# Kernel optimization log

Hardware: AMD Instinct MI355X
Metric: run time of the kernel (lower is better)

The kernel has to match this reference:

```python
import jax, jax.numpy as jnp
import numpy as np

OUT, IN, RANK = 4096, 4096, 1024
B, T = 4, 4096

def setup_inputs() -> dict:
    key = jax.random.key(0)
    kx, ku, ks, kv = jax.random.split(key, 4)
    x = jax.random.normal(kx, (B, T, IN), dtype=jnp.float32)
    # Orthonormal-ish factors scaled like SVD outputs
    U = jax.random.normal(ku, (OUT, RANK), dtype=jnp.float32) / np.sqrt(OUT)
    S = jax.random.uniform(ks, (RANK,), dtype=jnp.float32, minval=0.1, maxval=10.0)
    S = jnp.sort(S)[::-1]  # descending singular values
    V = jax.random.normal(kv, (IN, RANK), dtype=jnp.float32) / np.sqrt(IN)
    return {"x": x, "U": U, "S": S, "V": V}

def reference(x, U, S, V):
    # Faithful to torch: weight = U @ diag(S) @ V.T  (shape [out, in]),
    # then F.linear(x, weight) = x @ weight.T
    weight = (U * S[None, :]) @ V.T          # [out, in]
    return jnp.einsum('bti,oi->bto', x, weight)
```

## Files before the change

kernel.cpp:

```cpp
#include <hip/hip_runtime.h>


typedef __bf16 bf16;
typedef __bf16 bf16x4 __attribute__((ext_vector_type(4)));
typedef __bf16 bf16x8 __attribute__((ext_vector_type(8)));
typedef float  f32x4  __attribute__((ext_vector_type(4)));

#define M_DIM   16384
#define IN_DIM  4096
#define OUT_DIM 4096
#define RK_DIM  1024

__global__ __launch_bounds__(256)
void prep_kernel(const float* __restrict__ x, const float* __restrict__ U,
                 const float* __restrict__ S, const float* __restrict__ V,
                 bf16* __restrict__ xb, bf16* __restrict__ Ub,
                 bf16* __restrict__ VsT, int xblocks)
{
    __shared__ float tile[64][68];
    const int b = blockIdx.x;
    const int tid = threadIdx.x;

    if (b < xblocks) {
        const float4* xin = (const float4*)x;
        size_t base = (size_t)b * 2048 + tid;
        #pragma unroll
        for (int i = 0; i < 8; ++i) {
            float4 v = xin[base + (size_t)i * 256];
            bf16x4 o = { (bf16)v.x, (bf16)v.y, (bf16)v.z, (bf16)v.w };
            *(bf16x4*)&xb[(base + (size_t)i * 256) * 4] = o;
        }
    } else if (b < xblocks + 512) {
        const float4* uin = (const float4*)U;
        size_t base = (size_t)(b - xblocks) * 2048 + tid;
        #pragma unroll
        for (int i = 0; i < 8; ++i) {
            float4 v = uin[base + (size_t)i * 256];
            bf16x4 o = { (bf16)v.x, (bf16)v.y, (bf16)v.z, (bf16)v.w };
            *(bf16x4*)&Ub[(base + (size_t)i * 256) * 4] = o;
        }
    } else {
        const int vb   = b - (xblocks + 512);
        const int rblk = vb & 15;
        const int iblk = vb >> 4;
        const int r0 = rblk * 64, i0 = iblk * 64;

        const int tr  = tid >> 4;
        const int tc4 = (tid & 15) * 4;
        #pragma unroll
        for (int j = 0; j < 4; ++j) {
            float4 v = *(const float4*)&V[(size_t)(i0 + tr + j * 16) * RK_DIM + r0 + tc4];
            tile[tr + j * 16][tc4 + 0] = v.x;
            tile[tr + j * 16][tc4 + 1] = v.y;
            tile[tr + j * 16][tc4 + 2] = v.z;
            tile[tr + j * 16][tc4 + 3] = v.w;
        }
        __syncthreads();
        const int rr  = tid >> 2;
        const int ic0 = (tid & 3) * 16;
        const float s = S[r0 + rr];
        #pragma unroll
        for (int j = 0; j < 4; ++j) {
            bf16x4 o;
            #pragma unroll
            for (int q = 0; q < 4; ++q)
                o[q] = (bf16)(tile[ic0 + j * 4 + q][rr] * s);
            *(bf16x4*)&VsT[(size_t)(r0 + rr) * IN_DIM + i0 + ic0 + j * 4] = o;
        }
    }
}

__device__ __forceinline__ void gload16(const bf16* g, bf16* l)
{
    __builtin_amdgcn_global_load_lds(
        (const __attribute__((address_space(1))) void*)g,
        (__attribute__((address_space(3))) void*)l,
        16, 0, 0);
}

template <typename CT>
__global__ __launch_bounds__(256)
void gemm_bt_async(const bf16* __restrict__ A, const bf16* __restrict__ B,
                   CT* __restrict__ C, int M, int N, int K)
{
    __shared__ bf16 As[128][32];
    __shared__ bf16 Bs[128][32];

    const int tid  = threadIdx.x;
    const int lane = tid & 63;
    const int wave = tid >> 6;
    const int wrow = wave >> 1;
    const int wcol = wave & 1;
    const int n0 = blockIdx.x * 128;
    const int m0 = blockIdx.y * 128;

    f32x4 acc[4][4];
    #pragma unroll
    for (int mi = 0; mi < 4; ++mi)
        #pragma unroll
        for (int ni = 0; ni < 4; ++ni)
            acc[mi][ni] = (f32x4){0.f, 0.f, 0.f, 0.f};

    const int fr = lane & 15;
    const int kq = (lane >> 4) * 8;

    const int srow = lane >> 2;
    const int skc  = (lane & 3) * 8;

    for (int kk = 0; kk < K; kk += 32) {
        __syncthreads();
        #pragma unroll
        for (int i = 0; i < 2; ++i) {
            const int chunk = i * 4 + wave;
            const int row   = chunk * 16 + srow;
            gload16(&A[(size_t)(m0 + row) * K + kk + skc], &As[0][0] + chunk * 512);
            gload16(&B[(size_t)(n0 + row) * K + kk + skc], &Bs[0][0] + chunk * 512);
        }
        __syncthreads();

        bf16x8 af[4], bfg[4];
        #pragma unroll
        for (int i = 0; i < 4; ++i) {
            af[i]  = *(const bf16x8*)&As[wrow * 64 + i * 16 + fr][kq];
            bfg[i] = *(const bf16x8*)&Bs[wcol * 64 + i * 16 + fr][kq];
        }
        #pragma unroll
        for (int mi = 0; mi < 4; ++mi)
            #pragma unroll
            for (int ni = 0; ni < 4; ++ni)
                acc[mi][ni] = __builtin_amdgcn_mfma_f32_16x16x32_bf16(
                    af[mi], bfg[ni], acc[mi][ni], 0, 0, 0);
    }

    const int ccol  = n0 + wcol * 64 + fr;
    const int crow0 = m0 + wrow * 64 + (lane >> 4) * 4;
    #pragma unroll
    for (int mi = 0; mi < 4; ++mi)
        #pragma unroll
        for (int ni = 0; ni < 4; ++ni)
            #pragma unroll
            for (int r = 0; r < 4; ++r)
                C[(size_t)(crow0 + mi * 16 + r) * N + ccol + ni * 16] =
                    (CT)acc[mi][ni][r];
}

__global__ __launch_bounds__(256)
void gemm_bt_f32a(const float* __restrict__ A, const bf16* __restrict__ B,
                  bf16* __restrict__ C, int M, int N, int K)
{
    __shared__ bf16 As[128][40];
    __shared__ bf16 Bs[128][40];

    const int tid  = threadIdx.x;
    const int lane = tid & 63;
    const int wave = tid >> 6;
    const int wrow = wave >> 1;
    const int wcol = wave & 1;
    const int n0 = blockIdx.x * 128;
    const int m0 = blockIdx.y * 128;

    f32x4 acc[4][4];
    #pragma unroll
    for (int mi = 0; mi < 4; ++mi)
        #pragma unroll
        for (int ni = 0; ni < 4; ++ni)
            acc[mi][ni] = (f32x4){0.f, 0.f, 0.f, 0.f};

    const int fr = lane & 15;
    const int kq = (lane >> 4) * 8;

    for (int kk = 0; kk < K; kk += 32) {
        __syncthreads();
        #pragma unroll
        for (int i = 0; i < 4; ++i) {
            int c = tid + i * 256;
            int row = c >> 3, kc = (c & 7) * 4;
            float4 v = *(const float4*)&A[(size_t)(m0 + row) * K + kk + kc];
            bf16x4 o = { (bf16)v.x, (bf16)v.y, (bf16)v.z, (bf16)v.w };
            *(bf16x4*)&As[row][kc] = o;
        }
        #pragma unroll
        for (int i = 0; i < 2; ++i) {
            int c = tid + i * 256;
            int row = c >> 2, kc = (c & 3) * 8;
            *(bf16x8*)&Bs[row][kc] = *(const bf16x8*)&B[(size_t)(n0 + row) * K + kk + kc];
        }
        __syncthreads();

        bf16x8 af[4], bfg[4];
        #pragma unroll
        for (int i = 0; i < 4; ++i) {
            af[i]  = *(const bf16x8*)&As[wrow * 64 + i * 16 + fr][kq];
            bfg[i] = *(const bf16x8*)&Bs[wcol * 64 + i * 16 + fr][kq];
        }
        #pragma unroll
        for (int mi = 0; mi < 4; ++mi)
            #pragma unroll
            for (int ni = 0; ni < 4; ++ni)
                acc[mi][ni] = __builtin_amdgcn_mfma_f32_16x16x32_bf16(
                    af[mi], bfg[ni], acc[mi][ni], 0, 0, 0);
    }

    const int ccol  = n0 + wcol * 64 + fr;
    const int crow0 = m0 + wrow * 64 + (lane >> 4) * 4;
    #pragma unroll
    for (int mi = 0; mi < 4; ++mi)
        #pragma unroll
        for (int ni = 0; ni < 4; ++ni)
            #pragma unroll
            for (int r = 0; r < 4; ++r)
                C[(size_t)(crow0 + mi * 16 + r) * N + ccol + ni * 16] =
                    (bf16)acc[mi][ni][r];
}

extern "C" void kernel_launch(void* const* d_in, const int* in_sizes, int n_in,
                              void* d_out, int out_size, void* d_ws, size_t ws_size,
                              hipStream_t stream)
{
    const float* x = (const float*)d_in[0];
    const float* U = (const float*)d_in[1];
    const float* S = (const float*)d_in[2];
    const float* V = (const float*)d_in[3];
    float* out = (float*)d_out;

    const size_t SZ_XB  = (size_t)M_DIM * IN_DIM * 2;
    const size_t SZ_UB  = (size_t)OUT_DIM * RK_DIM * 2;
    const size_t SZ_VST = (size_t)RK_DIM * IN_DIM * 2;
    const size_t SZ_T   = (size_t)M_DIM * RK_DIM * 2;

    char* p = (char*)d_ws;
    const bool full = ws_size >= SZ_XB + SZ_UB + SZ_VST + SZ_T;
    bf16* xb = nullptr;
    if (full) { xb = (bf16*)p; p += SZ_XB; }
    bf16* Ub  = (bf16*)p; p += SZ_UB;
    bf16* VsT = (bf16*)p; p += SZ_VST;
    bf16* t   = (bf16*)p;

    const int xblocks = full ? 8192 : 0;
    prep_kernel<<<xblocks + 512 + 1024, 256, 0, stream>>>(
        x, U, S, V, full ? xb : Ub, Ub, VsT, xblocks);

    if (full)
        gemm_bt_async<bf16><<<dim3(RK_DIM / 128, M_DIM / 128), 256, 0, stream>>>(
            xb, VsT, t, M_DIM, RK_DIM, IN_DIM);
    else
        gemm_bt_f32a<<<dim3(RK_DIM / 128, M_DIM / 128), 256, 0, stream>>>(
            x, VsT, t, M_DIM, RK_DIM, IN_DIM);

    gemm_bt_async<float><<<dim3(OUT_DIM / 128, M_DIM / 128), 256, 0, stream>>>(
        t, Ub, out, M_DIM, OUT_DIM, RK_DIM);
}
```

Before: 871.1 us.

## Replace GEMM with 256x256 eight-wave double-buffered pipelined MFMA kernel

Both bf16 GEMMs move from a 128x128 tile kernel with 4 waves and a sync-load-compute loop to a 256x256 tile kernel with 8 waves and K-steps of 64. The new kernel double-buffers LDS, issues async global-to-LDS loads for upcoming tiles between MFMA phases, and uses an XOR swizzle to avoid LDS bank conflicts. It also sets wave priority around the MFMA bursts. The aim is to hide memory latency behind compute and raise arithmetic intensity. In exchange it uses 128KB of LDS and many accumulator registers, which limits occupancy, and the hand-written vmcnt waits are fragile.

```diff
diff --git a/kernel.cpp b/kernel.cpp
--- a/kernel.cpp
+++ b/kernel.cpp
@@ -79,12 +79,175 @@
 }
 
 template <typename CT>
+__global__ __launch_bounds__(512)
+void gemm_bt_8p(const bf16* __restrict__ A, const bf16* __restrict__ B,
+                CT* __restrict__ C, int M, int N, int K)
+{
+    __shared__ bf16 lds[2][2][2][8192];
+
+    const int tid  = threadIdx.x;
+    const int lane = tid & 63;
+    const int wave = tid >> 6;
+    const int wrow = wave >> 2;
+    const int wcol = wave & 3;
+    const int n0 = blockIdx.x * 256;
+    const int m0 = blockIdx.y * 256;
+    const int NT = K >> 6;
+
+    const int srow8  = lane >> 3;
+    const int colswz = ((lane & 7) * 8) ^ (((lane >> 4) & 1) * 8)
+                                        ^ (((lane >> 5) & 1) * 16);
+
+    const int fr   = lane & 15;
+    const int kq2  = (lane >> 4) * 16;
+    const int x45  = (fr & 6) << 3;
+    const int x6   = (fr & 8) << 3;
+    const int koffe[2] = { ((kq2 ^ x45) + (0  ^ x6)) >> 1,
+                           ((kq2 ^ x45) + (64 ^ x6)) >> 1 };
+
+    f32x4 acc[8][4];
+    #pragma unroll
+    for (int mi = 0; mi < 8; ++mi)
+        #pragma unroll
+        for (int ni = 0; ni < 4; ++ni)
+            acc[mi][ni] = (f32x4){0.f, 0.f, 0.f, 0.f};
+
+    auto STAGE = [&](const bf16* __restrict__ G, int g0, int tile, int op, int half) {
+        bf16* dst = &lds[tile & 1][op][half][wave * 1024];
+        #pragma unroll
+        for (int i = 0; i < 2; ++i) {
+            const int row = g0 + half * 128 + wave * 16 + i * 8 + srow8;
+            const bf16* src = G + (size_t)row * K + tile * 64 + (colswz ^ (i * 32));
+            gload16(src, dst + i * 512);
+        }
+    };
+
+    STAGE(A, m0, 0, 0, 0); STAGE(A, m0, 0, 0, 1);
+    STAGE(B, n0, 0, 1, 0); STAGE(B, n0, 0, 1, 1);
+    if (NT > 1) {
+        STAGE(A, m0, 1, 0, 0); STAGE(A, m0, 1, 0, 1); STAGE(B, n0, 1, 1, 0);
+        asm volatile("s_waitcnt vmcnt(6)" ::: "memory");
+    } else {
+        asm volatile("s_waitcnt vmcnt(0)" ::: "memory");
+    }
+    __builtin_amdgcn_s_barrier();
+
+    bf16x8 af[4][2], bv[4][2];
+
+    for (int t = 0; t < NT; ++t) {
+        const int cbuf = t & 1;
+        const bf16* aB = &lds[cbuf][0][wrow][fr * 64];
+        const bf16* bB = &lds[cbuf][1][wcol >> 1][(wcol & 1) * 4096 + fr * 64];
+
+        #pragma unroll
+        for (int q = 0; q < 4; ++q)
+            #pragma unroll
+            for (int h = 0; h < 2; ++h)
+                af[q][h] = *(const bf16x8*)(aB + q * 1024 + koffe[h]);
+        #pragma unroll
+        for (int n = 0; n < 2; ++n)
+            #pragma unroll
+            for (int h = 0; h < 2; ++h)
+                bv[n][h] = *(const bf16x8*)(bB + n * 1024 + koffe[h]);
+        if (t + 1 < NT) STAGE(B, n0, t + 1, 1, 1);
+        __builtin_amdgcn_s_barrier();
+        asm volatile("s_waitcnt lgkmcnt(0)" ::: "memory");
+        __builtin_amdgcn_sched_barrier(0);
+        __builtin_amdgcn_s_setprio(1);
+        #pragma unroll
+        for (int q = 0; q < 4; ++q)
+            #pragma unroll
+            for (int n = 0; n < 2; ++n)
+                #pragma unroll
+                for (int h = 0; h < 2; ++h)
+                    acc[q][n] = __builtin_amdgcn_mfma_f32_16x16x32_bf16(
+                        af[q][h], bv[n][h], acc[q][n], 0, 0, 0);
+        __builtin_amdgcn_s_setprio(0);
+        __builtin_amdgcn_s_barrier();
+
+        #pragma unroll
+        for (int n = 2; n < 4; ++n)
+            #pragma unroll
+            for (int h = 0; h < 2; ++h)
+                bv[n][h] = *(const bf16x8*)(bB + n * 1024 + koffe[h]);
+        __builtin_amdgcn_s_barrier();
+        asm volatile("s_waitcnt lgkmcnt(0)" ::: "memory");
+        __builtin_amdgcn_sched_barrier(0);
+        __builtin_amdgcn_s_setprio(1);
+        #pragma unroll
+        for (int q = 0; q < 4; ++q)
+            #pragma unroll
+            for (int n = 2; n < 4; ++n)
+                #pragma unroll
+                for (int h = 0; h < 2; ++h)
+                    acc[q][n] = __builtin_amdgcn_mfma_f32_16x16x32_bf16(
+                        af[q][h], bv[n][h], acc[q][n], 0, 0, 0);
+        __builtin_amdgcn_s_setprio(0);
+        __builtin_amdgcn_s_barrier();
+
+        #pragma unroll
+        for (int q = 0; q < 4; ++q)
+            #pragma unroll
+            for (int h = 0; h < 2; ++h)
+                af[q][h] = *(const bf16x8*)(aB + (4 + q) * 1024 + koffe[h]);
+        if (t + 2 < NT) STAGE(B, n0, t + 2, 1, 0);
+        __builtin_amdgcn_s_barrier();
+        asm volatile("s_waitcnt lgkmcnt(0)" ::: "memory");
+        __builtin_amdgcn_sched_barrier(0);
+        __builtin_amdgcn_s_setprio(1);
+        #pragma unroll
+        for (int q = 0; q < 4; ++q)
+            #pragma unroll
+            for (int n = 2; n < 4; ++n)
+                #pragma unroll
+                for (int h = 0; h < 2; ++h)
+                    acc[4 + q][n] = __builtin_amdgcn_mfma_f32_16x16x32_bf16(
+                        af[q][h], bv[n][h], acc[4 + q][n], 0, 0, 0);
+        __builtin_amdgcn_s_setprio(0);
+        __builtin_amdgcn_s_barrier();
+
+        if (t + 2 < NT) {
+            STAGE(A, m0, t + 2, 0, 0);
+            STAGE(A, m0, t + 2, 0, 1);
+        }
+        __builtin_amdgcn_s_barrier();
+        asm volatile("s_waitcnt lgkmcnt(0)" ::: "memory");
+        __builtin_amdgcn_sched_barrier(0);
+        __builtin_amdgcn_s_setprio(1);
+        #pragma unroll
+        for (int q = 0; q < 4; ++q)
+            #pragma unroll
+            for (int n = 0; n < 2; ++n)
+                #pragma unroll
+                for (int h = 0; h < 2; ++h)
+                    acc[4 + q][n] = __builtin_amdgcn_mfma_f32_16x16x32_bf16(
+                        af[q][h], bv[n][h], acc[4 + q][n], 0, 0, 0);
+        __builtin_amdgcn_s_setprio(0);
+        if (t + 2 < NT)
+            asm volatile("s_waitcnt vmcnt(6)" ::: "memory");
+        else if (t + 1 < NT)
+            asm volatile("s_waitcnt vmcnt(0)" ::: "memory");
+        __builtin_amdgcn_s_barrier();
+    }
+
+    const int ccol  = n0 + wcol * 64 + fr;
+    const int crow0 = m0 + wrow * 128 + (lane >> 4) * 4;
+    #pragma unroll
+    for (int mi = 0; mi < 8; ++mi)
+        #pragma unroll
+        for (int ni = 0; ni < 4; ++ni)
+            #pragma unroll
+            for (int r = 0; r < 4; ++r)
+                C[(size_t)(crow0 + mi * 16 + r) * N + ccol + ni * 16] =
+                    (CT)acc[mi][ni][r];
+}
+
 __global__ __launch_bounds__(256)
-void gemm_bt_async(const bf16* __restrict__ A, const bf16* __restrict__ B,
-                   CT* __restrict__ C, int M, int N, int K)
-{
-    __shared__ bf16 As[128][32];
-    __shared__ bf16 Bs[128][32];
+void gemm_bt_f32a(const float* __restrict__ A, const bf16* __restrict__ B,
+                  bf16* __restrict__ C, int M, int N, int K)
+{
+    __shared__ bf16 As[128][40];
+    __shared__ bf16 Bs[128][40];
 
     const int tid  = threadIdx.x;
     const int lane = tid & 63;
@@ -104,71 +267,6 @@
     const int fr = lane & 15;
     const int kq = (lane >> 4) * 8;
 
-    const int srow = lane >> 2;
-    const int skc  = (lane & 3) * 8;
-
-    for (int kk = 0; kk < K; kk += 32) {
-        __syncthreads();
-        #pragma unroll
-        for (int i = 0; i < 2; ++i) {
-            const int chunk = i * 4 + wave;
-            const int row   = chunk * 16 + srow;
-            gload16(&A[(size_t)(m0 + row) * K + kk + skc], &As[0][0] + chunk * 512);
-            gload16(&B[(size_t)(n0 + row) * K + kk + skc], &Bs[0][0] + chunk * 512);
-        }
-        __syncthreads();
-
-        bf16x8 af[4], bfg[4];
-        #pragma unroll
-        for (int i = 0; i < 4; ++i) {
-            af[i]  = *(const bf16x8*)&As[wrow * 64 + i * 16 + fr][kq];
-            bfg[i] = *(const bf16x8*)&Bs[wcol * 64 + i * 16 + fr][kq];
-        }
-        #pragma unroll
-        for (int mi = 0; mi < 4; ++mi)
-            #pragma unroll
-            for (int ni = 0; ni < 4; ++ni)
-                acc[mi][ni] = __builtin_amdgcn_mfma_f32_16x16x32_bf16(
-                    af[mi], bfg[ni], acc[mi][ni], 0, 0, 0);
-    }
-
-    const int ccol  = n0 + wcol * 64 + fr;
-    const int crow0 = m0 + wrow * 64 + (lane >> 4) * 4;
-    #pragma unroll
-    for (int mi = 0; mi < 4; ++mi)
-        #pragma unroll
-        for (int ni = 0; ni < 4; ++ni)
-            #pragma unroll
-            for (int r = 0; r < 4; ++r)
-                C[(size_t)(crow0 + mi * 16 + r) * N + ccol + ni * 16] =
-                    (CT)acc[mi][ni][r];
-}
-
-__global__ __launch_bounds__(256)
-void gemm_bt_f32a(const float* __restrict__ A, const bf16* __restrict__ B,
-                  bf16* __restrict__ C, int M, int N, int K)
-{
-    __shared__ bf16 As[128][40];
-    __shared__ bf16 Bs[128][40];
-
-    const int tid  = threadIdx.x;
-    const int lane = tid & 63;
-    const int wave = tid >> 6;
-    const int wrow = wave >> 1;
-    const int wcol = wave & 1;
-    const int n0 = blockIdx.x * 128;
-    const int m0 = blockIdx.y * 128;
-
-    f32x4 acc[4][4];
-    #pragma unroll
-    for (int mi = 0; mi < 4; ++mi)
-        #pragma unroll
-        for (int ni = 0; ni < 4; ++ni)
-            acc[mi][ni] = (f32x4){0.f, 0.f, 0.f, 0.f};
-
-    const int fr = lane & 15;
-    const int kq = (lane >> 4) * 8;
-
     for (int kk = 0; kk < K; kk += 32) {
         __syncthreads();
         #pragma unroll
@@ -241,12 +339,12 @@
         x, U, S, V, full ? xb : Ub, Ub, VsT, xblocks);
 
     if (full)
-        gemm_bt_async<bf16><<<dim3(RK_DIM / 128, M_DIM / 128), 256, 0, stream>>>(
+        gemm_bt_8p<bf16><<<dim3(RK_DIM / 256, M_DIM / 256), 512, 0, stream>>>(
             xb, VsT, t, M_DIM, RK_DIM, IN_DIM);
     else
         gemm_bt_f32a<<<dim3(RK_DIM / 128, M_DIM / 128), 256, 0, stream>>>(
             x, VsT, t, M_DIM, RK_DIM, IN_DIM);
 
-    gemm_bt_async<float><<<dim3(OUT_DIM / 128, M_DIM / 128), 256, 0, stream>>>(
+    gemm_bt_8p<float><<<dim3(OUT_DIM / 256, M_DIM / 256), 512, 0, stream>>>(
         t, Ub, out, M_DIM, OUT_DIM, RK_DIM);
 }
```

Result: faster. 706.4 us (-18.9%).
